# Performance work log

Hardware: AMD Instinct MI355X
Metric: run time of the kernel (lower is better)

## Reference

```python
import jax, jax.numpy as jnp
import numpy as np


def setup_inputs() -> dict:
    key = jax.random.key(0)
    ks = jax.random.split(key, 7)
    B, T, I, H, O = 64, 2048, 32, 256, 32
    s = 0.05
    return {
        "x": jax.random.normal(ks[0], (B, T, I), dtype=jnp.float32),
        "W_ih": jax.random.normal(ks[1], (4 * H, I), dtype=jnp.float32) * s,
        "W_hh": jax.random.normal(ks[2], (4 * H, H), dtype=jnp.float32) * s,
        "b_ih": jax.random.normal(ks[3], (4 * H,), dtype=jnp.float32) * s,
        "b_hh": jax.random.normal(ks[4], (4 * H,), dtype=jnp.float32) * s,
        "fc_w": jax.random.normal(ks[5], (O, H), dtype=jnp.float32) * s,
        "fc_b": jax.random.normal(ks[6], (O,), dtype=jnp.float32) * s,
    }


def _lstm(x, W_ih, W_hh, b_ih, b_hh):
    # x: [B,T,I]; PyTorch gate order: i, f, g, o stacked along 4H axis.
    B = x.shape[0]
    H = W_hh.shape[1]
    # Precompute input contributions for all timesteps in one GEMM: [B,T,4H]
    xg = jnp.einsum('bti,gi->btg', x, W_ih) + b_ih + b_hh

    def step(carry, xg_t):
        h, c = carry  # [B,H] each
        gates = xg_t + h @ W_hh.T  # [B,4H]
        i, f, g, o = jnp.split(gates, 4, axis=-1)
        i = jax.nn.sigmoid(i)
        f = jax.nn.sigmoid(f)
        g = jnp.tanh(g)
        o = jax.nn.sigmoid(o)
        c = f * c + i * g
        h = o * jnp.tanh(c)
        return (h, c), h

    h0 = jnp.zeros((B, H), dtype=x.dtype)
    (_, _), hs = jax.lax.scan(step, (h0, h0), jnp.swapaxes(xg, 0, 1))
    return jnp.swapaxes(hs, 0, 1)  # [B,T,H]


def reference(x, W_ih, W_hh, b_ih, b_hh, fc_w, fc_b):
    out = _lstm(x, W_ih, W_hh, b_ih, b_hh)          # [B,T,H]
    # Conv1d(H, O, kernel_size=1) over channel dim == pointwise linear.
    return jnp.einsum('bth,oh->bto', out, fc_w) + fc_b  # [B,T,O]
```

## Files before the change

### kernel.cpp

```cpp
#include <hip/hip_runtime.h>
#include <cstdint>


#define B_  64
#define T_  2048
#define I_  32
#define H_  256
#define O_  32

typedef unsigned int v4u __attribute__((ext_vector_type(4)));
typedef _Float16 h2_t __attribute__((ext_vector_type(2)));

#if __has_builtin(__builtin_amdgcn_sdot4)
__device__ __forceinline__ int dot4(int a, int b, int c) {
    return __builtin_amdgcn_sdot4(a, b, c, false);
}
#else
__device__ __forceinline__ int dot4(int a, int b, int c) {
    c += (int)(int8_t)(a)        * (int)(int8_t)(b);
    c += (int)(int8_t)(a >> 8)   * (int)(int8_t)(b >> 8);
    c += (int)(int8_t)(a >> 16)  * (int)(int8_t)(b >> 16);
    c += (int)(int8_t)(a >> 24)  * (int)(int8_t)(b >> 24);
    return c;
}
#endif

__device__ __forceinline__ float fdot2h(h2_t a, h2_t b, float c) {
#if __has_builtin(__builtin_amdgcn_fdot2)
    return __builtin_amdgcn_fdot2(a, b, c, false);
#else
    return c + (float)a[0] * (float)b[0] + (float)a[1] * (float)b[1];
#endif
}

__device__ __forceinline__ float wave64_max_bcast(float v) {
    int t;
    t = __builtin_amdgcn_update_dpp(__float_as_int(v), __float_as_int(v), 0x111, 0xf, 0xf, false);
    v = fmaxf(v, __int_as_float(t));
    t = __builtin_amdgcn_update_dpp(__float_as_int(v), __float_as_int(v), 0x112, 0xf, 0xf, false);
    v = fmaxf(v, __int_as_float(t));
    t = __builtin_amdgcn_update_dpp(__float_as_int(v), __float_as_int(v), 0x114, 0xf, 0xf, false);
    v = fmaxf(v, __int_as_float(t));
    t = __builtin_amdgcn_update_dpp(__float_as_int(v), __float_as_int(v), 0x118, 0xf, 0xf, false);
    v = fmaxf(v, __int_as_float(t));
    t = __builtin_amdgcn_update_dpp(__float_as_int(v), __float_as_int(v), 0x142, 0xa, 0xf, false);
    v = fmaxf(v, __int_as_float(t));
    t = __builtin_amdgcn_update_dpp(__float_as_int(v), __float_as_int(v), 0x143, 0xc, 0xf, false);
    v = fmaxf(v, __int_as_float(t));
    return __int_as_float(__builtin_amdgcn_readlane(__float_as_int(v), 63));
}

__device__ __forceinline__ float sum8(float v) {
    int t;
    t = __builtin_amdgcn_update_dpp(0, __float_as_int(v), 0x111, 0xf, 0xf, true); v += __int_as_float(t);
    t = __builtin_amdgcn_update_dpp(0, __float_as_int(v), 0x112, 0xf, 0xf, true); v += __int_as_float(t);
    t = __builtin_amdgcn_update_dpp(0, __float_as_int(v), 0x114, 0xf, 0xf, true); v += __int_as_float(t);
    return v;
}

#define QW_OFF   0
#define WIH_OFF  262144
#define S1_OFF   327680
#define BIAS_OFF 331776
#define XH_OFF   335872

__device__ __forceinline__ uint32_t pack_q(int q0, int q1, int q2, int q3) {
    return  ((uint32_t)(uint8_t)(int8_t)q0)
          | (((uint32_t)(uint8_t)(int8_t)q1) << 8)
          | (((uint32_t)(uint8_t)(int8_t)q2) << 16)
          | (((uint32_t)(uint8_t)(int8_t)q3) << 24);
}

__device__ __forceinline__ int clamp127(int v) {
    return v < -127 ? -127 : (v > 127 ? 127 : v);
}

__global__ __launch_bounds__(64) void prep_w(
    const float* __restrict__ Whh, const float* __restrict__ Wih,
    const float* __restrict__ bih, const float* __restrict__ bhh,
    uint32_t* __restrict__ qw4, uint32_t* __restrict__ wih4,
    float* __restrict__ s1v, float* __restrict__ biasv)
{
    const int gr = blockIdx.x;
    const int c  = threadIdx.x;
    const int j  = gr >> 8;
    const int r  = gr & 255;

    const float4 wv = ((const float4*)(Whh + gr * H_))[c];
    float m = fmaxf(fmaxf(fabsf(wv.x), fabsf(wv.y)), fmaxf(fabsf(wv.z), fabsf(wv.w)));
    #pragma unroll
    for (int s = 1; s < 64; s <<= 1) m = fmaxf(m, __shfl_xor(m, s, 64));
    const float S1 = fmaxf(m, 1e-20f) / 127.f;
    const float r1 = 1.f / S1;

    {
        const int d = j * 64 + c;
        qw4[(d >> 2) * 1024 + r * 4 + (d & 3)] = pack_q(
            clamp127((int)rintf(wv.x * r1)), clamp127((int)rintf(wv.y * r1)),
            clamp127((int)rintf(wv.z * r1)), clamp127((int)rintf(wv.w * r1)));
    }
    if (c < 16) {
        union { uint32_t u; h2_t h; } z;
        z.h[0] = (_Float16)Wih[gr * I_ + 2 * c];
        z.h[1] = (_Float16)Wih[gr * I_ + 2 * c + 1];
        const int dd = j * 16 + c;
        wih4[(dd >> 2) * 1024 + r * 4 + (dd & 3)] = z.u;
    }
    if (c == 0) { s1v[gr] = S1; biasv[gr] = bih[gr] + bhh[gr]; }
}

__global__ __launch_bounds__(256) void prep_xh(
    const float* __restrict__ x, uint32_t* __restrict__ xh)
{
    const int i = blockIdx.x * 256 + threadIdx.x;
    const float2 v = ((const float2*)x)[i];
    union { uint32_t u; h2_t h; } z;
    z.h[0] = (_Float16)v.x; z.h[1] = (_Float16)v.y;
    xh[i] = z.u;
}

__global__ __launch_bounds__(256, 1) void lstm_main(
    const uint32_t* __restrict__ qw4, const uint32_t* __restrict__ wih4,
    const float* __restrict__ s1v, const float* __restrict__ biasv,
    const uint32_t* __restrict__ xh, const float* __restrict__ fcw,
    const float* __restrict__ fcb, float* __restrict__ out)
{
    const int b  = blockIdx.x;
    const int r  = threadIdx.x;
    const int ln = r & 63;
    const int wv = r >> 6;

    __shared__ uint32_t hqb[2][64];
    __shared__ __align__(16) float hscb[2][4];
    __shared__ uint32_t hfb[2][128];

    v4u w4[64];
    #pragma unroll
    for (int d4 = 0; d4 < 64; d4++) w4[d4] = ((const v4u*)qw4)[d4 * 256 + r];
    v4u wx[16];
    #pragma unroll
    for (int d4 = 0; d4 < 16; d4++) wx[d4] = ((const v4u*)wih4)[d4 * 256 + r];
    float S1j[4], bj[4];
    #pragma unroll
    for (int j = 0; j < 4; j++) { S1j[j] = s1v[j * 256 + r]; bj[j] = biasv[j * 256 + r]; }

    const int o_ = r >> 3, ks = r & 7;
    h2_t fw[16];
    {
        const float* fr = fcw + o_ * H_ + ks * 32;
        #pragma unroll
        for (int i = 0; i < 16; i++) {
            h2_t p; p[0] = (_Float16)fr[2 * i]; p[1] = (_Float16)fr[2 * i + 1];
            fw[i] = p;
        }
    }
    const float fcb_v = fcb[o_];

    if (r < 4) hscb[1][r] = 0.f;
    __syncthreads();

    const uint32_t* xb   = xh + (size_t)(b * T_) * 16;
    float*          outb = out + (size_t)(b * T_) * O_;

    float c_state = 0.f;

    for (int t = 0; t < T_; t++) {
        const int pb = (t & 1) ^ 1, cb = t & 1;

        const v4u* xv = (const v4u*)(xb + (size_t)t * 16);
        const v4u x0 = xv[0], x1 = xv[1], x2 = xv[2], x3 = xv[3];

        const v4u*   hqv = (const v4u*)&hqb[pb][0];
        const float4 scv = *(const float4*)&hscb[pb][0];
        const float  scar[4] = { scv.x, scv.y, scv.z, scv.w };

        float a0 = 0.f, a1 = 0.f, a2 = 0.f, a3 = 0.f;
        #pragma unroll
        for (int g = 0; g < 4; g++) {
            v4u hg[4];
            #pragma unroll
            for (int q = 0; q < 4; q++) hg[q] = hqv[g * 4 + q];
            int i0 = 0, i1 = 0, i2 = 0, i3 = 0;
            #pragma unroll
            for (int q = 0; q < 4; q++) {
                #pragma unroll
                for (int e = 0; e < 4; e++) {
                    const int hv = (int)hg[q][e];
                    i0 = dot4((int)w4[ 0 + g * 4 + q][e], hv, i0);
                    i1 = dot4((int)w4[16 + g * 4 + q][e], hv, i1);
                    i2 = dot4((int)w4[32 + g * 4 + q][e], hv, i2);
                    i3 = dot4((int)w4[48 + g * 4 + q][e], hv, i3);
                }
            }
            a0 = fmaf((float)i0, scar[g], a0);
            a1 = fmaf((float)i1, scar[g], a1);
            a2 = fmaf((float)i2, scar[g], a2);
            a3 = fmaf((float)i3, scar[g], a3);
        }

        if (t > 0) {
            const v4u* hfv = (const v4u*)&hfb[pb][0];
            v4u fh[4];
            #pragma unroll
            for (int i = 0; i < 4; i++) fh[i] = hfv[ks * 4 + i];
            float acc = 0.f;
            #pragma unroll
            for (int i = 0; i < 16; i++) {
                union { uint32_t u; h2_t h; } z;
                z.u = fh[i >> 2][i & 3];
                acc = fdot2h(fw[i], z.h, acc);
            }
            acc = sum8(acc);
            if (ks == 7) outb[(t - 1) * O_ + o_] = acc + fcb_v;
        }

        float xd0 = 0.f, xd1 = 0.f, xd2 = 0.f, xd3 = 0.f;
        {
            const v4u xg4[4] = { x0, x1, x2, x3 };
            #pragma unroll
            for (int d4 = 0; d4 < 4; d4++) {
                #pragma unroll
                for (int e = 0; e < 4; e++) {
                    union { uint32_t u; h2_t h; } zx, z0, z1, z2, z3;
                    zx.u = xg4[d4][e];
                    z0.u = wx[ 0 + d4][e]; xd0 = fdot2h(z0.h, zx.h, xd0);
                    z1.u = wx[ 4 + d4][e]; xd1 = fdot2h(z1.h, zx.h, xd1);
                    z2.u = wx[ 8 + d4][e]; xd2 = fdot2h(z2.h, zx.h, xd2);
                    z3.u = wx[12 + d4][e]; xd3 = fdot2h(z3.h, zx.h, xd3);
                }
            }
        }

        const float g0 = fmaf(a0, S1j[0], xd0 + bj[0]);
        const float g1 = fmaf(a1, S1j[1], xd1 + bj[1]);
        const float g2 = fmaf(a2, S1j[2], xd2 + bj[2]);
        const float g3 = fmaf(a3, S1j[3], xd3 + bj[3]);
        const float i_ = 1.f / (1.f + __expf(-g0));
        const float f_ = 1.f / (1.f + __expf(-g1));
        const float gg = 2.f / (1.f + __expf(-2.f * g2)) - 1.f;
        const float oo = 1.f / (1.f + __expf(-g3));
        c_state = f_ * c_state + i_ * gg;
        const float tc = 2.f / (1.f + __expf(-2.f * c_state)) - 1.f;
        const float hval = oo * tc;

        float m = wave64_max_bcast(fabsf(hval));
        m = fmaxf(m, 1e-12f);
        const int q = clamp127((int)rintf(hval * (127.f / m)));
        ((char*)&hqb[cb][0])[r] = (char)(int8_t)q;
        if (ln == 0) hscb[cb][wv] = m * (1.f / 127.f);
        ((_Float16*)&hfb[cb][0])[r] = (_Float16)hval;

        asm volatile("s_waitcnt lgkmcnt(0)" ::: "memory");
        __builtin_amdgcn_s_barrier();
    }

    {
        const int pb = (T_ - 1) & 1;
        const v4u* hfv = (const v4u*)&hfb[pb][0];
        v4u fh[4];
        #pragma unroll
        for (int i = 0; i < 4; i++) fh[i] = hfv[ks * 4 + i];
        float acc = 0.f;
        #pragma unroll
        for (int i = 0; i < 16; i++) {
            union { uint32_t u; h2_t h; } z;
            z.u = fh[i >> 2][i & 3];
            acc = fdot2h(fw[i], z.h, acc);
        }
        acc = sum8(acc);
        if (ks == 7) outb[(T_ - 1) * O_ + o_] = acc + fcb_v;
    }
}

extern "C" void kernel_launch(void* const* d_in, const int* in_sizes, int n_in,
                              void* d_out, int out_size, void* d_ws, size_t ws_size,
                              hipStream_t stream) {
    const float* x    = (const float*)d_in[0];
    const float* Wih  = (const float*)d_in[1];
    const float* Whh  = (const float*)d_in[2];
    const float* bih  = (const float*)d_in[3];
    const float* bhh  = (const float*)d_in[4];
    const float* fcw  = (const float*)d_in[5];
    const float* fcb  = (const float*)d_in[6];
    float* out = (float*)d_out;

    char* ws = (char*)d_ws;
    uint32_t* qw4   = (uint32_t*)(ws + QW_OFF);
    uint32_t* wih4  = (uint32_t*)(ws + WIH_OFF);
    float*    s1v   = (float*)(ws + S1_OFF);
    float*    biasv = (float*)(ws + BIAS_OFF);
    uint32_t* xh    = (uint32_t*)(ws + XH_OFF);

    prep_w<<<1024, 64, 0, stream>>>(Whh, Wih, bih, bhh, qw4, wih4, s1v, biasv);
    prep_xh<<<(B_ * T_ * 16) / 256, 256, 0, stream>>>(x, xh);
    lstm_main<<<B_, 256, 0, stream>>>(qw4, wih4, s1v, biasv, xh, fcw, fcb, out);
}
```

Before: 3.410 ms.

## Batch LSTM recurrence across 16 sequences per block using int8 MFMA

Replaces the one-block-per-sequence dot4 recurrence with a 4-block design where each 512-thread block processes 16 batch rows and computes h@W_hh with int8 16x16x64 MFMA. Hidden states are requantized per row each step through a swizzled shared-memory buffer and atomicMax. The input projection moves into its own precompute kernel, and the output projection moves into a separate fc kernel that reads an fp16 hidden-state history buffer. This trades per-sequence parallelism (only 4 blocks active) and a large workspace for matrix-core throughput. It falls back to the old path when the workspace is too small.

```diff
diff --git a/kernel.cpp b/kernel.cpp
--- a/kernel.cpp
+++ b/kernel.cpp
@@ -7,7 +7,10 @@
 #define I_  32
 #define H_  256
 #define O_  32
-
+#define MB  16
+#define NBLK 4
+
+typedef int v4i __attribute__((ext_vector_type(4)));
 typedef unsigned int v4u __attribute__((ext_vector_type(4)));
 typedef _Float16 h2_t __attribute__((ext_vector_type(2)));
 
@@ -58,11 +61,31 @@
     return v;
 }
 
-#define QW_OFF   0
-#define WIH_OFF  262144
-#define S1_OFF   327680
-#define BIAS_OFF 331776
-#define XH_OFF   335872
+__device__ __forceinline__ float row16_max(float v) {
+    int t;
+    t = __builtin_amdgcn_update_dpp(__float_as_int(v), __float_as_int(v), 0x111, 0xf, 0xf, false);
+    v = fmaxf(v, __int_as_float(t));
+    t = __builtin_amdgcn_update_dpp(__float_as_int(v), __float_as_int(v), 0x112, 0xf, 0xf, false);
+    v = fmaxf(v, __int_as_float(t));
+    t = __builtin_amdgcn_update_dpp(__float_as_int(v), __float_as_int(v), 0x114, 0xf, 0xf, false);
+    v = fmaxf(v, __int_as_float(t));
+    t = __builtin_amdgcn_update_dpp(__float_as_int(v), __float_as_int(v), 0x118, 0xf, 0xf, false);
+    v = fmaxf(v, __int_as_float(t));
+    return v;
+}
+
+#define WQ_OFF    0
+#define S1_OFF    262144
+#define BIAS_OFF  266240
+#define WIHH_OFF  270336
+#define XH_OFF    335872
+#define XGA_OFF   8724480
+#define HIST_OFF  277159936
+#define WS_NEED   344268800ULL
+#define FQW_OFF   0
+#define FWIH_OFF  262144
+#define FS1_OFF   327680
+#define FBIAS_OFF 331776
 
 __device__ __forceinline__ uint32_t pack_q(int q0, int q1, int q2, int q3) {
     return  ((uint32_t)(uint8_t)(int8_t)q0)
@@ -75,7 +98,268 @@
     return v < -127 ? -127 : (v > 127 ? 127 : v);
 }
 
-__global__ __launch_bounds__(64) void prep_w(
+__global__ __launch_bounds__(256) void prep_xh(
+    const float* __restrict__ x, uint32_t* __restrict__ xh)
+{
+    const int i = blockIdx.x * 256 + threadIdx.x;
+    const float2 v = ((const float2*)x)[i];
+    union { uint32_t u; h2_t h; } z;
+    z.h[0] = (_Float16)v.x; z.h[1] = (_Float16)v.y;
+    xh[i] = z.u;
+}
+
+__global__ __launch_bounds__(64) void prep_wq(
+    const float* __restrict__ Whh, const float* __restrict__ Wih,
+    const float* __restrict__ bih, const float* __restrict__ bhh,
+    uint32_t* __restrict__ wq, float* __restrict__ s1p,
+    float* __restrict__ biasp, uint32_t* __restrict__ wihh)
+{
+    const int gr = blockIdx.x;
+    const int j  = threadIdx.x;
+    const int g  = gr >> 8, r = gr & 255;
+    const int c  = ((r >> 4) << 6) | (g << 4) | (r & 15);
+
+    const float4 wv = ((const float4*)(Whh + gr * H_))[j];
+    float m = fmaxf(fmaxf(fabsf(wv.x), fabsf(wv.y)), fmaxf(fabsf(wv.z), fabsf(wv.w)));
+    #pragma unroll
+    for (int s = 1; s < 64; s <<= 1) m = fmaxf(m, __shfl_xor(m, s, 64));
+    const float S1 = fmaxf(m, 1e-20f) / 127.f;
+    const float r1 = 1.f / S1;
+    wq[c * 64 + j] = pack_q(
+        clamp127((int)rintf(wv.x * r1)), clamp127((int)rintf(wv.y * r1)),
+        clamp127((int)rintf(wv.z * r1)), clamp127((int)rintf(wv.w * r1)));
+    if (j < 16) {
+        union { uint32_t u; h2_t h; } z;
+        z.h[0] = (_Float16)Wih[gr * I_ + 2 * j];
+        z.h[1] = (_Float16)Wih[gr * I_ + 2 * j + 1];
+        wihh[c * 16 + j] = z.u;
+    }
+    if (j == 0) { s1p[c] = S1; biasp[c] = bih[gr] + bhh[gr]; }
+}
+
+__global__ __launch_bounds__(512) void prep_xg(
+    const uint32_t* __restrict__ xh, const uint32_t* __restrict__ wihh,
+    const float* __restrict__ biasp, uint32_t* __restrict__ xga)
+{
+    const int bx = blockIdx.x;
+    const int blk = bx >> 11, t = bx & 2047;
+    const int tid = threadIdx.x;
+    const int wv = tid >> 6, l = tid & 63, lq = l >> 4, lo = l & 15;
+
+    uint32_t outw[16];
+    #pragma unroll
+    for (int reg = 0; reg < 4; reg++) {
+        const int b = blk * MB + lq * 4 + reg;
+        const uint32_t* xr = xh + ((size_t)b * T_ + t) * 16;
+        uint32_t xd[16];
+        #pragma unroll
+        for (int d = 0; d < 16; d++) xd[d] = xr[d];
+        #pragma unroll
+        for (int np = 0; np < 4; np++) {
+            float acc2[2];
+            #pragma unroll
+            for (int hh = 0; hh < 2; hh++) {
+                const int nt = np * 2 + hh;
+                const int c = wv * 128 + nt * 16 + lo;
+                const uint32_t* wr = wihh + c * 16;
+                float acc = biasp[c];
+                #pragma unroll
+                for (int d = 0; d < 16; d++) {
+                    union { uint32_t u; h2_t h; } zw, zx;
+                    zw.u = wr[d]; zx.u = xd[d];
+                    acc = fdot2h(zw.h, zx.h, acc);
+                }
+                acc2[hh] = acc;
+            }
+            union { uint32_t u; h2_t h; } zo;
+            zo.h[0] = (_Float16)acc2[0]; zo.h[1] = (_Float16)acc2[1];
+            outw[reg * 4 + np] = zo.u;
+        }
+    }
+    uint32_t* dst = xga + ((size_t)bx * 512 + tid) * 16;
+    #pragma unroll
+    for (int d = 0; d < 16; d++) dst[d] = outw[d];
+}
+
+__global__ __launch_bounds__(512, 2) void lstm_mfma(
+    const uint32_t* __restrict__ wq, const float* __restrict__ s1p,
+    const uint32_t* __restrict__ xga, _Float16* __restrict__ hist)
+{
+    const int blk = blockIdx.x;
+    const int tid = threadIdx.x;
+    const int wv = tid >> 6, l = tid & 63, lq = l >> 4, lo = l & 15;
+
+    __shared__ char  Ab[2][4096];
+    __shared__ int   shmax[2][16];
+    __shared__ float shsc[2][16];
+
+    v4i  wB[8][4];
+    float s1c[8];
+    #pragma unroll
+    for (int nt = 0; nt < 8; nt++) {
+        const int c = wv * 128 + nt * 16 + lo;
+        s1c[nt] = s1p[c];
+        #pragma unroll
+        for (int kt = 0; kt < 4; kt++)
+            wB[nt][kt] = *(const v4i*)(wq + (size_t)c * 64 + kt * 16 + lq * 4);
+    }
+
+    {
+        uint32_t* a0 = (uint32_t*)&Ab[0][0];
+        a0[tid] = 0; a0[tid + 512] = 0;
+        if (tid < 16) { shmax[0][tid] = 0; shmax[1][tid] = 0; shsc[0][tid] = 0.f; }
+    }
+    __syncthreads();
+
+    float cst[4][2];
+    #pragma unroll
+    for (int reg = 0; reg < 4; reg++) { cst[reg][0] = 0.f; cst[reg][1] = 0.f; }
+
+    size_t hbase[4][2];
+    #pragma unroll
+    for (int reg = 0; reg < 4; reg++)
+        #pragma unroll
+        for (int rr = 0; rr < 2; rr++)
+            hbase[reg][rr] = ((size_t)(blk * MB + lq * 4 + reg) * T_) * 256
+                           + (size_t)(wv * 32 + rr * 16 + lo);
+
+    const uint32_t* xgb = xga + (size_t)blk * T_ * 8192 + (size_t)tid * 16;
+
+    v4u xgv[4];
+    {
+        const v4u* xp = (const v4u*)xgb;
+        xgv[0] = xp[0]; xgv[1] = xp[1]; xgv[2] = xp[2]; xgv[3] = xp[3];
+    }
+
+    for (int t = 0; t < T_; t++) {
+        const int rb = t & 1, wb = rb ^ 1;
+
+        float shp[4];
+        #pragma unroll
+        for (int reg = 0; reg < 4; reg++) shp[reg] = shsc[rb][lq * 4 + reg];
+
+        v4i af[4];
+        #pragma unroll
+        for (int kt = 0; kt < 4; kt++)
+            af[kt] = *(const v4i*)&Ab[rb][lo * 256 + (((kt * 4 + lq) ^ lo) << 4)];
+
+        v4i C[8];
+        #pragma unroll
+        for (int nt = 0; nt < 8; nt++) {
+            v4i acc = {0, 0, 0, 0};
+            #pragma unroll
+            for (int kt = 0; kt < 4; kt++)
+                acc = __builtin_amdgcn_mfma_i32_16x16x64_i8(af[kt], wB[nt][kt], acc, 0, 0, 0);
+            C[nt] = acc;
+        }
+
+        float hv[4][2];
+        #pragma unroll
+        for (int reg = 0; reg < 4; reg++) {
+            const float sp = shp[reg];
+            #pragma unroll
+            for (int rr = 0; rr < 2; rr++) {
+                float ga[4];
+                #pragma unroll
+                for (int g = 0; g < 4; g++) {
+                    const int nt = rr * 4 + g;
+                    const int d  = reg * 4 + (nt >> 1);
+                    const uint32_t u = xgv[d >> 2][d & 3] >> (16 * (nt & 1));
+                    union { unsigned short s; _Float16 h; } ux;
+                    ux.s = (unsigned short)(u & 0xffffu);
+                    ga[g] = fmaf((float)C[nt][reg], s1c[nt] * sp, (float)ux.h);
+                }
+                const float i_ = 1.f / (1.f + __expf(-ga[0]));
+                const float f_ = 1.f / (1.f + __expf(-ga[1]));
+                const float g_ = 2.f / (1.f + __expf(-2.f * ga[2])) - 1.f;
+                const float o_ = 1.f / (1.f + __expf(-ga[3]));
+                const float cs = f_ * cst[reg][rr] + i_ * g_;
+                cst[reg][rr] = cs;
+                const float tc = 2.f / (1.f + __expf(-2.f * cs)) - 1.f;
+                const float h = o_ * tc;
+                hv[reg][rr] = h;
+                hist[hbase[reg][rr] + (size_t)t * 256] = (_Float16)h;
+            }
+        }
+
+        {
+            const int tn = (t + 1 < T_) ? (t + 1) : t;
+            const v4u* xp = (const v4u*)(xgb + (size_t)tn * 8192);
+            xgv[0] = xp[0]; xgv[1] = xp[1]; xgv[2] = xp[2]; xgv[3] = xp[3];
+        }
+
+        #pragma unroll
+        for (int reg = 0; reg < 4; reg++) {
+            float vm = fmaxf(fabsf(hv[reg][0]), fabsf(hv[reg][1]));
+            vm = row16_max(vm);
+            if (lo == 15) atomicMax(&shmax[wb][lq * 4 + reg], __float_as_int(vm));
+        }
+
+        asm volatile("s_waitcnt lgkmcnt(0)" ::: "memory");
+        __builtin_amdgcn_s_barrier();
+
+        float rq[4];
+        #pragma unroll
+        for (int reg = 0; reg < 4; reg++) {
+            const float mm = fmaxf(__int_as_float(shmax[wb][lq * 4 + reg]), 1e-12f);
+            rq[reg] = 127.f / mm;
+        }
+        if (tid < 16) {
+            shsc[wb][tid] = fmaxf(__int_as_float(shmax[wb][tid]), 1e-12f) * (1.f / 127.f);
+            shmax[rb][tid] = 0;
+        }
+        #pragma unroll
+        for (int reg = 0; reg < 4; reg++) {
+            const int b = lq * 4 + reg;
+            #pragma unroll
+            for (int rr = 0; rr < 2; rr++) {
+                const int q = clamp127((int)rintf(hv[reg][rr] * rq[reg]));
+                const int r = wv * 32 + rr * 16 + lo;
+                Ab[wb][b * 256 + ((((r >> 4) ^ b) & 15) << 4) + (r & 15)] = (char)(int8_t)q;
+            }
+        }
+
+        asm volatile("s_waitcnt lgkmcnt(0)" ::: "memory");
+        __builtin_amdgcn_s_barrier();
+    }
+}
+
+__global__ __launch_bounds__(256) void fc_out(
+    const uint32_t* __restrict__ hist, const float* __restrict__ fcw,
+    const float* __restrict__ fcb, float* __restrict__ out)
+{
+    const int tid = threadIdx.x;
+    const int o_ = tid >> 3, ks = tid & 7;
+    h2_t fw[16];
+    {
+        const float* fr = fcw + o_ * H_ + ks * 32;
+        #pragma unroll
+        for (int i = 0; i < 16; i++) {
+            h2_t p; p[0] = (_Float16)fr[2 * i]; p[1] = (_Float16)fr[2 * i + 1];
+            fw[i] = p;
+        }
+    }
+    const float fcbv = fcb[o_];
+    const size_t base = (size_t)blockIdx.x * 64;
+    for (int i = 0; i < 64; i++) {
+        const size_t ro = base + i;
+        const v4u* hp = (const v4u*)(hist + ro * 128 + ks * 16);
+        v4u fh[4];
+        #pragma unroll
+        for (int k = 0; k < 4; k++) fh[k] = hp[k];
+        float acc = 0.f;
+        #pragma unroll
+        for (int k = 0; k < 16; k++) {
+            union { uint32_t u; h2_t h; } z;
+            z.u = fh[k >> 2][k & 3];
+            acc = fdot2h(fw[k], z.h, acc);
+        }
+        acc = sum8(acc);
+        if (ks == 7) out[ro * 32 + o_] = acc + fcbv;
+    }
+}
+
+__global__ __launch_bounds__(64) void prep_w_fb(
     const float* __restrict__ Whh, const float* __restrict__ Wih,
     const float* __restrict__ bih, const float* __restrict__ bhh,
     uint32_t* __restrict__ qw4, uint32_t* __restrict__ wih4,
@@ -92,7 +376,6 @@
     for (int s = 1; s < 64; s <<= 1) m = fmaxf(m, __shfl_xor(m, s, 64));
     const float S1 = fmaxf(m, 1e-20f) / 127.f;
     const float r1 = 1.f / S1;
-
     {
         const int d = j * 64 + c;
         qw4[(d >> 2) * 1024 + r * 4 + (d & 3)] = pack_q(
@@ -109,17 +392,7 @@
     if (c == 0) { s1v[gr] = S1; biasv[gr] = bih[gr] + bhh[gr]; }
 }
 
-__global__ __launch_bounds__(256) void prep_xh(
-    const float* __restrict__ x, uint32_t* __restrict__ xh)
-{
-    const int i = blockIdx.x * 256 + threadIdx.x;
-    const float2 v = ((const float2*)x)[i];
-    union { uint32_t u; h2_t h; } z;
-    z.h[0] = (_Float16)v.x; z.h[1] = (_Float16)v.y;
-    xh[i] = z.u;
-}
-
-__global__ __launch_bounds__(256, 1) void lstm_main(
+__global__ __launch_bounds__(256, 1) void lstm_fb(
     const uint32_t* __restrict__ qw4, const uint32_t* __restrict__ wih4,
     const float* __restrict__ s1v, const float* __restrict__ biasv,
     const uint32_t* __restrict__ xh, const float* __restrict__ fcw,
@@ -185,11 +458,11 @@
             for (int q = 0; q < 4; q++) {
                 #pragma unroll
                 for (int e = 0; e < 4; e++) {
-                    const int hv = (int)hg[q][e];
-                    i0 = dot4((int)w4[ 0 + g * 4 + q][e], hv, i0);
-                    i1 = dot4((int)w4[16 + g * 4 + q][e], hv, i1);
-                    i2 = dot4((int)w4[32 + g * 4 + q][e], hv, i2);
-                    i3 = dot4((int)w4[48 + g * 4 + q][e], hv, i3);
+                    const int hvv = (int)hg[q][e];
+                    i0 = dot4((int)w4[ 0 + g * 4 + q][e], hvv, i0);
+                    i1 = dot4((int)w4[16 + g * 4 + q][e], hvv, i1);
+                    i2 = dot4((int)w4[32 + g * 4 + q][e], hvv, i2);
+                    i3 = dot4((int)w4[48 + g * 4 + q][e], hvv, i3);
                 }
             }
             a0 = fmaf((float)i0, scar[g], a0);
@@ -285,13 +558,29 @@
     float* out = (float*)d_out;
 
     char* ws = (char*)d_ws;
-    uint32_t* qw4   = (uint32_t*)(ws + QW_OFF);
-    uint32_t* wih4  = (uint32_t*)(ws + WIH_OFF);
-    float*    s1v   = (float*)(ws + S1_OFF);
-    float*    biasv = (float*)(ws + BIAS_OFF);
-    uint32_t* xh    = (uint32_t*)(ws + XH_OFF);
-
-    prep_w<<<1024, 64, 0, stream>>>(Whh, Wih, bih, bhh, qw4, wih4, s1v, biasv);
-    prep_xh<<<(B_ * T_ * 16) / 256, 256, 0, stream>>>(x, xh);
-    lstm_main<<<B_, 256, 0, stream>>>(qw4, wih4, s1v, biasv, xh, fcw, fcb, out);
-}
+    uint32_t* xh = (uint32_t*)(ws + XH_OFF);
+
+    if (ws_size >= WS_NEED) {
+        uint32_t*  wq    = (uint32_t*)(ws + WQ_OFF);
+        float*     s1p   = (float*)(ws + S1_OFF);
+        float*     biasp = (float*)(ws + BIAS_OFF);
+        uint32_t*  wihh  = (uint32_t*)(ws + WIHH_OFF);
+        uint32_t*  xga   = (uint32_t*)(ws + XGA_OFF);
+        _Float16*  hist  = (_Float16*)(ws + HIST_OFF);
+
+        prep_wq<<<1024, 64, 0, stream>>>(Whh, Wih, bih, bhh, wq, s1p, biasp, wihh);
+        prep_xh<<<(B_ * T_ * 16) / 256, 256, 0, stream>>>(x, xh);
+        prep_xg<<<NBLK * T_, 512, 0, stream>>>(xh, wihh, biasp, xga);
+        lstm_mfma<<<NBLK, 512, 0, stream>>>(wq, s1p, xga, hist);
+        fc_out<<<(B_ * T_) / 64, 256, 0, stream>>>((const uint32_t*)hist, fcw, fcb, out);
+    } else {
+        uint32_t* qw4   = (uint32_t*)(ws + FQW_OFF);
+        uint32_t* wih4  = (uint32_t*)(ws + FWIH_OFF);
+        float*    s1v   = (float*)(ws + FS1_OFF);
+        float*    biasv = (float*)(ws + FBIAS_OFF);
+
+        prep_w_fb<<<1024, 64, 0, stream>>>(Whh, Wih, bih, bhh, qw4, wih4, s1v, biasv);
+        prep_xh<<<(B_ * T_ * 16) / 256, 256, 0, stream>>>(x, xh);
+        lstm_fb<<<B_, 256, 0, stream>>>(qw4, wih4, s1v, biasv, xh, fcw, fcb, out);
+    }
+}
```

Result: no change. 3.435 ms (+0.7%).
